# Kernel optimization log

Hardware: AMD Instinct MI355X
Metric: run time of the kernel (lower is better)

The kernel has to match this reference:

```python
import jax, jax.numpy as jnp
import numpy as np

B, T, C = 2, 2048, 1024
H, DH = 16, 64          # n_heads = d_model // 64
WIN = 256               # sliding window size
K = 32                  # n_oscillators
DFF = 4096              # d_ff_hidden
NEG = -1e9


def setup_inputs() -> dict:
    key = jax.random.key(0)
    ks = jax.random.split(key, 16)
    sC = 1.0 / np.sqrt(C)
    sF = 1.0 / np.sqrt(DFF)
    sK = 1.0 / np.sqrt(K)
    return {
        "x": jax.random.normal(ks[0], (B, T, C), jnp.float32),
        "norm1_w": jnp.ones((C,), jnp.float32),
        "qkv_w": jax.random.normal(ks[1], (3 * C, C), jnp.float32) * sC,
        "qkv_b": jnp.zeros((3 * C,), jnp.float32),
        "proj_w": jax.random.normal(ks[2], (C, C), jnp.float32) * sC,
        "proj_b": jnp.zeros((C,), jnp.float32),
        "gate_w": jax.random.normal(ks[3], (1, C), jnp.float32) * 0.01,
        "gate_b": jnp.zeros((1,), jnp.float32),
        "trn_win": jax.random.normal(ks[4], (K, C), jnp.float32) * sC,
        "trn_wout": jax.random.normal(ks[5], (C, K), jnp.float32) * sK,
        "trn_gate_w": jax.random.normal(ks[6], (K, C), jnp.float32) * sC,
        "trn_gate_b": jnp.zeros((K,), jnp.float32),
        "trn_a_logit": jax.random.normal(ks[7], (K,), jnp.float32),
        "trn_theta": jax.random.uniform(ks[8], (K,), jnp.float32, 0.0, np.pi),
        "trn_res_scale": jnp.asarray(0.1, jnp.float32),
        "norm2_w": jnp.ones((C,), jnp.float32),
        "ffn_gate_w": jax.random.normal(ks[9], (DFF, C), jnp.float32) * sC,
        "ffn_up_w": jax.random.normal(ks[10], (DFF, C), jnp.float32) * sC,
        "ffn_down_w": jax.random.normal(ks[11], (C, DFF), jnp.float32) * sF,
    }


def _rms(z, w, eps=1e-6):
    return z * jax.lax.rsqrt(jnp.mean(z * z, axis=-1, keepdims=True) + eps) * w


def reference(x, norm1_w, qkv_w, qkv_b, proj_w, proj_b, gate_w, gate_b,
              trn_win, trn_wout, trn_gate_w, trn_gate_b, trn_a_logit,
              trn_theta, trn_res_scale, norm2_w, ffn_gate_w, ffn_up_w,
              ffn_down_w):
    h = _rms(x, norm1_w)

    # ---- windowed causal attention (dense mask, as in the original) ----
    qkv = h @ qkv_w.T + qkv_b                       # [B,T,3C]
    q, k, v = jnp.split(qkv, 3, axis=-1)
    heads = lambda t: t.reshape(B, T, H, DH).transpose(0, 2, 1, 3)  # [B,H,T,DH]
    q, k, v = heads(q), heads(k), heads(v)
    row = jnp.arange(T)[:, None]
    col = jnp.arange(T)[None, :]
    mask = jnp.where((col <= row) & (col >= row - WIN + 1), 0.0, NEG).astype(x.dtype)
    scores = jnp.einsum('bhqd,bhkd->bhqk', q, k) / jnp.sqrt(jnp.asarray(DH, x.dtype))
    attn = jax.nn.softmax(scores + mask, axis=-1)
    ao = jnp.einsum('bhqk,bhkd->bhqd', attn, v).transpose(0, 2, 1, 3).reshape(B, T, C)
    ao = ao @ proj_w.T + proj_b

    # ---- temporal resonance branch: K damped rotating oscillators ----
    u = h @ trn_win.T                               # [B,T,K] drive
    a = jax.nn.sigmoid(trn_a_logit)                 # amplitude in (0,1) (amplitude_max=1)
    ct, st = jnp.cos(trn_theta), jnp.sin(trn_theta)

    def step(carry, ut):
        sr, si = carry
        nsr = a * (ct * sr - st * si) + ut
        nsi = a * (st * sr + ct * si)
        return (nsr, nsi), nsr

    init = (jnp.zeros((B, K), x.dtype), jnp.zeros((B, K), x.dtype))
    _, ys = jax.lax.scan(step, init, u.transpose(1, 0, 2))  # ys: [T,B,K]
    y = ys.transpose(1, 0, 2)                                # [B,T,K]
    tg = jax.nn.sigmoid(h @ trn_gate_w.T + trn_gate_b)
    trn_out = ((tg * y) @ trn_wout.T) * trn_res_scale        # [B,T,C]

    # ---- sigmoid gate mix + residual ----
    g = jax.nn.sigmoid(h @ gate_w.T + gate_b)       # [B,T,1]
    x = x + g * ao + (1.0 - g) * trn_out

    # ---- SwiGLU FFN ----
    h2 = _rms(x, norm2_w)
    ffn = (jax.nn.silu(h2 @ ffn_gate_w.T) * (h2 @ ffn_up_w.T)) @ ffn_down_w.T
    return x + ffn
```

## Files before the change

### kernel.cpp

```cpp
#include <hip/hip_runtime.h>


typedef unsigned short u16;
typedef unsigned short u16x8 __attribute__((ext_vector_type(8)));
typedef __bf16 bf16x8 __attribute__((ext_vector_type(8)));
typedef float f32x4 __attribute__((ext_vector_type(4)));

#define DI static __device__ __forceinline__

DI u16 f2b(float f){
  union { float f; unsigned u; } v; v.f = f;
  unsigned r = v.u + 0x7FFFu + ((v.u >> 16) & 1u);
  return (u16)(r >> 16);
}
DI float b2f(u16 b){
  union { unsigned u; float f; } v; v.u = ((unsigned)b) << 16; return v.f;
}
DI u16x8 ld8(const u16* p){ return *(const u16x8*)p; }

DI f32x4 MFMA16(u16x8 a, u16x8 b, f32x4 c){
  return __builtin_amdgcn_mfma_f32_16x16x32_bf16(
      __builtin_bit_cast(bf16x8, a), __builtin_bit_cast(bf16x8, b), c, 0, 0, 0);
}

DI void async16(const void* g, void* l){
  void* gg = const_cast<void*>(g);
  __builtin_amdgcn_global_load_lds(
      (__attribute__((address_space(1))) void*)gg,
      (__attribute__((address_space(3))) void*)l, 16, 0, 0);
}

__global__ __launch_bounds__(256) void convert_w(
    const float* __restrict__ qkvw, const float* __restrict__ projw,
    const float* __restrict__ fgw, const float* __restrict__ fuw,
    const float* __restrict__ fdw, const float* __restrict__ twin,
    const float* __restrict__ tgw, const float* __restrict__ twout,
    u16* __restrict__ dst)
{
  size_t i = (size_t)blockIdx.x * 256 + threadIdx.x;
  if (i >= 4235264u) return;
  size_t e = i * 4;
  float4 v;
  if (e < 3145728u)        v = *(const float4*)(qkvw + e);
  else if (e < 3276800u){
    size_t i2 = e - 3145728u;
    int row = (int)(i2 >> 10), c = (int)(i2 & 1023);
    if (row < 32)      v = *(const float4*)(twin + row * 1024 + c);
    else if (row < 64) v = *(const float4*)(tgw + (row - 32) * 1024 + c);
    else               v = make_float4(0.f, 0.f, 0.f, 0.f);
  }
  else if (e < 4325376u)   v = *(const float4*)(projw + (e - 3276800u));
  else if (e < 12713984u){
    size_t i2 = e - 4325376u;
    int row = (int)(i2 >> 10), c = (int)(i2 & 1023);
    int G = row >> 5, j = row & 31;
    const float* src = (j < 16) ? fgw : fuw;
    v = *(const float4*)(src + (size_t)(G * 16 + (j & 15)) * 1024 + c);
  }
  else if (e < 16908288u)  v = *(const float4*)(fdw + (e - 12713984u));
  else                     v = *(const float4*)(twout + (e - 16908288u));
  uint2 p;
  p.x = (unsigned)f2b(v.x) | ((unsigned)f2b(v.y) << 16);
  p.y = (unsigned)f2b(v.z) | ((unsigned)f2b(v.w) << 16);
  *(uint2*)(dst + e) = p;
}

__global__ __launch_bounds__(256) void rmsnorm_gate(
    const float* __restrict__ x, const float* __restrict__ w,
    const float* __restrict__ gw, const float* __restrict__ gb,
    u16* __restrict__ h, float* __restrict__ g)
{
  const int row = blockIdx.x, tid = threadIdx.x;
  const int wave = tid >> 6, lane = tid & 63;
  __shared__ float sb[8];
  float4 xv = ((const float4*)(x + (size_t)row * 1024))[tid];
  float ss = xv.x*xv.x + xv.y*xv.y + xv.z*xv.z + xv.w*xv.w;
#pragma unroll
  for (int m = 32; m; m >>= 1) ss += __shfl_xor(ss, m);
  if (lane == 0) sb[wave] = ss;
  __syncthreads();
  float rstd = rsqrtf((sb[0]+sb[1]+sb[2]+sb[3]) * (1.f/1024.f) + 1e-6f);
  float4 wv = ((const float4*)w)[tid];
  float h0 = xv.x*rstd*wv.x, h1 = xv.y*rstd*wv.y;
  float h2v = xv.z*rstd*wv.z, h3 = xv.w*rstd*wv.w;
  uint2 pk;
  pk.x = (unsigned)f2b(h0) | ((unsigned)f2b(h1) << 16);
  pk.y = (unsigned)f2b(h2v) | ((unsigned)f2b(h3) << 16);
  ((uint2*)(h + (size_t)row * 1024))[tid] = pk;
  float4 gv = ((const float4*)gw)[tid];
  float gd = h0*gv.x + h1*gv.y + h2v*gv.z + h3*gv.w;
#pragma unroll
  for (int m = 32; m; m >>= 1) gd += __shfl_xor(gd, m);
  if (lane == 0) sb[4 + wave] = gd;
  __syncthreads();
  if (tid == 0) g[row] = 1.f / (1.f + __expf(-(sb[4]+sb[5]+sb[6]+sb[7] + gb[0])));
}

__global__ __launch_bounds__(256) void reduce_mix_norm(
    const u16* __restrict__ part, const float* __restrict__ x,
    const u16* __restrict__ trn, const float* __restrict__ g,
    const float* __restrict__ pb, const float* __restrict__ n2w,
    float* __restrict__ out, u16* __restrict__ h2)
{
  const int row = blockIdx.x, tid = threadIdx.x;
  const int wave = tid >> 6, lane = tid & 63;
  __shared__ float sb[4];
  const size_t ro = (size_t)row * 1024;
  uint2 a0 = ((const uint2*)(part + ro))[tid];
  uint2 a1 = ((const uint2*)(part + 4194304 + ro))[tid];
  float4 bb = ((const float4*)pb)[tid];
  float4 xv = ((const float4*)(x + ro))[tid];
  uint2 tz = ((const uint2*)(trn + ro))[tid];
  float gg = g[row];
  float p00 = b2f((u16)a0.x), p01 = b2f((u16)(a0.x >> 16));
  float p02 = b2f((u16)a0.y), p03 = b2f((u16)(a0.y >> 16));
  float p10 = b2f((u16)a1.x), p11 = b2f((u16)(a1.x >> 16));
  float p12 = b2f((u16)a1.y), p13 = b2f((u16)(a1.y >> 16));
  float t0 = b2f((u16)tz.x), t1 = b2f((u16)(tz.x >> 16));
  float t2 = b2f((u16)tz.y), t3 = b2f((u16)(tz.y >> 16));
  float m0 = xv.x + gg*(p00+p10+bb.x) + (1.f-gg)*t0;
  float m1 = xv.y + gg*(p01+p11+bb.y) + (1.f-gg)*t1;
  float m2 = xv.z + gg*(p02+p12+bb.z) + (1.f-gg)*t2;
  float m3 = xv.w + gg*(p03+p13+bb.w) + (1.f-gg)*t3;
  float4 mo; mo.x = m0; mo.y = m1; mo.z = m2; mo.w = m3;
  ((float4*)(out + ro))[tid] = mo;
  float ss = m0*m0 + m1*m1 + m2*m2 + m3*m3;
#pragma unroll
  for (int m = 32; m; m >>= 1) ss += __shfl_xor(ss, m);
  if (lane == 0) sb[wave] = ss;
  __syncthreads();
  float rstd = rsqrtf((sb[0]+sb[1]+sb[2]+sb[3]) * (1.f/1024.f) + 1e-6f);
  float4 wv = ((const float4*)n2w)[tid];
  uint2 pk;
  pk.x = (unsigned)f2b(m0*rstd*wv.x) | ((unsigned)f2b(m1*rstd*wv.y) << 16);
  pk.y = (unsigned)f2b(m2*rstd*wv.z) | ((unsigned)f2b(m3*rstd*wv.w) << 16);
  ((uint2*)(h2 + ro))[tid] = pk;
}

__global__ __launch_bounds__(256) void reduce_down(
    const u16* __restrict__ part, float* __restrict__ out)
{
  size_t i = (size_t)blockIdx.x * 256 + threadIdx.x;
  uint2 a0 = ((const uint2*)part)[i];
  uint2 a1 = ((const uint2*)(part + 4194304))[i];
  float4 xv = ((float4*)out)[i];
  float4 o;
  o.x = xv.x + b2f((u16)a0.x) + b2f((u16)a1.x);
  o.y = xv.y + b2f((u16)(a0.x >> 16)) + b2f((u16)(a1.x >> 16));
  o.z = xv.z + b2f((u16)a0.y) + b2f((u16)a1.y);
  o.w = xv.w + b2f((u16)(a0.y >> 16)) + b2f((u16)(a1.y >> 16));
  ((float4*)out)[i] = o;
}

template<int MODE, bool WIDE>
__global__ __launch_bounds__(256) void gemm_bt(
    const u16* __restrict__ A, const u16* __restrict__ B,
    float* __restrict__ outF, float* __restrict__ outF2, u16* __restrict__ outB,
    const float* __restrict__ bias, const float* __restrict__ auxF,
    int M, int N, int K)
{
  __shared__ __align__(16) u16 sA[2][128 * 32];
  __shared__ __align__(16) u16 sB[2][128 * 32];
  const int tid = threadIdx.x;
  const int wave = tid >> 6, lane = tid & 63;
  const int lr = lane & 15, lq = lane >> 4;
  const int m0 = blockIdx.x * 128, n0 = blockIdx.y * 128;
  const int wm = (wave & 1) * 64, wn = (wave >> 1) * 64;
  const int ks = K / (int)gridDim.z;
  const int kbeg = (int)blockIdx.z * ks, kend = kbeg + ks;
  f32x4 acc[4][4] = {};
  const int srow = wave * 16 + (lane >> 2);
  const int scol = (lane & 3) * 8;
  const u16* gA = A + (size_t)(m0 + srow) * K + scol;
  const u16* gB = B + (size_t)(n0 + srow) * K + scol;
  u16* lA0 = &sA[0][(wave * 16) * 32];
  u16* lA1 = &sA[0][(64 + wave * 16) * 32];
  u16* lB0 = &sB[0][(wave * 16) * 32];
  u16* lB1 = &sB[0][(64 + wave * 16) * 32];
  const size_t K64 = (size_t)64 * K;
  const int BUF = 128 * 32;

  if (WIDE){
    for (int k0 = kbeg; k0 < kend; k0 += 64){
      async16(gA + k0,            lA0);
      async16(gA + K64 + k0,      lA1);
      async16(gB + k0,            lB0);
      async16(gB + K64 + k0,      lB1);
      async16(gA + k0 + 32,       lA0 + BUF);
      async16(gA + K64 + k0 + 32, lA1 + BUF);
      async16(gB + k0 + 32,       lB0 + BUF);
      async16(gB + K64 + k0 + 32, lB1 + BUF);
      __syncthreads();
      u16x8 af[4], bf[4];
#pragma unroll
      for (int i = 0; i < 4; i++) af[i] = ld8(&sA[0][(wm + i*16 + lr)*32 + lq*8]);
#pragma unroll
      for (int i = 0; i < 4; i++) bf[i] = ld8(&sB[0][(wn + i*16 + lr)*32 + lq*8]);
#pragma unroll
      for (int mi = 0; mi < 4; mi++)
#pragma unroll
        for (int ni = 0; ni < 4; ni++)
          acc[mi][ni] = MFMA16(af[mi], bf[ni], acc[mi][ni]);
#pragma unroll
      for (int i = 0; i < 4; i++) af[i] = ld8(&sA[1][(wm + i*16 + lr)*32 + lq*8]);
#pragma unroll
      for (int i = 0; i < 4; i++) bf[i] = ld8(&sB[1][(wn + i*16 + lr)*32 + lq*8]);
#pragma unroll
      for (int mi = 0; mi < 4; mi++)
#pragma unroll
        for (int ni = 0; ni < 4; ni++)
          acc[mi][ni] = MFMA16(af[mi], bf[ni], acc[mi][ni]);
      __syncthreads();
    }
  } else {
    for (int k0 = kbeg; k0 < kend; k0 += 32){
      async16(gA + k0,       lA0);
      async16(gA + K64 + k0, lA1);
      async16(gB + k0,       lB0);
      async16(gB + K64 + k0, lB1);
      __syncthreads();
      u16x8 af[4], bf[4];
#pragma unroll
      for (int i = 0; i < 4; i++) af[i] = ld8(&sA[0][(wm + i*16 + lr)*32 + lq*8]);
#pragma unroll
      for (int i = 0; i < 4; i++) bf[i] = ld8(&sB[0][(wn + i*16 + lr)*32 + lq*8]);
#pragma unroll
      for (int mi = 0; mi < 4; mi++)
#pragma unroll
        for (int ni = 0; ni < 4; ni++)
          acc[mi][ni] = MFMA16(af[mi], bf[ni], acc[mi][ni]);
      __syncthreads();
    }
  }

  if (MODE == 7){
    const int cb = ((n0 + wn) >> 1) + lr;
#pragma unroll
    for (int mi = 0; mi < 4; mi++){
      const int row = m0 + wm + mi*16 + lq*4;
#pragma unroll
      for (int p = 0; p < 2; p++){
        const int col = cb + p*16;
#pragma unroll
        for (int r = 0; r < 4; r++){
          float gv = acc[mi][2*p][r], uv = acc[mi][2*p+1][r];
          float rv = gv / (1.f + __expf(-gv)) * uv;
          outB[(size_t)(row + r) * (N >> 1) + col] = f2b(rv);
        }
      }
    }
    return;
  }

  float scale6 = 0.f;
  if (MODE == 6) scale6 = auxF[0];

#pragma unroll
  for (int mi = 0; mi < 4; mi++){
    const int row = m0 + wm + mi*16 + lq*4;
#pragma unroll
    for (int ni = 0; ni < 4; ni++){
      const int col = n0 + wn + ni*16 + lr;
#pragma unroll
      for (int r = 0; r < 4; r++){
        const int rr = row + r;
        float v = acc[mi][ni][r];
        if (MODE == 0){
          if (n0 < 3072){
            outB[(size_t)rr * 3072 + col] = f2b(v + bias[col]);
          } else {
            int c2 = col - 3072;
            int bb = rr >> 11, tt = rr & 2047;
            if (c2 < 32) outF[((size_t)bb * 32 + c2) * 2048 + tt] = v;
            else if (c2 < 64)
              outF2[(size_t)rr * 32 + (c2 - 32)] =
                  1.f / (1.f + __expf(-(v + auxF[c2 - 32])));
          }
        } else if (MODE == 6){
          outB[(size_t)rr * N + col] = f2b(v * scale6);
        } else if (MODE == 9){
          outB[(size_t)blockIdx.z * (size_t)M + (size_t)rr * N + col] = f2b(v);
        }
      }
    }
  }
}

__global__ __launch_bounds__(256) void attn_win(
    const u16* __restrict__ qkv, u16* __restrict__ ao)
{
  const int blk = blockIdx.x;
  const int tile = blk & 31, hh = (blk >> 5) & 15, b = blk >> 9;
  const int t0 = tile * 64;
  const int tid = threadIdx.x, wave = tid >> 6, lane = tid & 63;
  const int lr = lane & 15, lq = lane >> 4;
  const int qt = t0 + wave * 16;
  __shared__ __align__(16) u16 sVt[64 * 40];
  __shared__ __align__(16) u16 sP[4][16 * 32];

  const u16* base = qkv + (size_t)b * 2048 * 3072 + hh * 64;
  const u16* qrow = base + (size_t)(qt + lr) * 3072 + lq * 8;
  u16x8 qf0 = ld8(qrow), qf1 = ld8(qrow + 32);
  const u16* kbase = base + 1024;
  const u16* vbase = base + 2048;

  f32x4 o0 = {0,0,0,0}, o1 = {0,0,0,0}, o2 = {0,0,0,0}, o3 = {0,0,0,0};
  float lsum[4] = {0.f, 0.f, 0.f, 0.f};
  const float c1 = 0.125f * 1.44269504088896f;

  const int kb = (t0 >= 256) ? (t0 - 256) : 0;
  const int ntl = (t0 + 64 - kb) >> 5;
  for (int it = 0; it < ntl; ++it){
    const int kt = kb + it * 32;
    __syncthreads();
    {
      const int key = tid & 31, dseg = tid >> 5;
      const u16* gv = vbase + (size_t)(kt + key) * 3072 + dseg * 8;
      u16x8 v0 = ld8(gv);
#pragma unroll
      for (int j = 0; j < 8; j++)
        sVt[(dseg*8 + j) * 40 + key] = v0[j];
    }
    __syncthreads();
    const bool active = (kt < qt + 16) && (kt + 286 >= qt);
    if (!active) continue;

    f32x4 s0 = {0,0,0,0}, s1 = {0,0,0,0};
    {
      const u16* kr = kbase + (size_t)(kt + lr) * 3072 + lq * 8;
      u16x8 k00 = ld8(kr), k01 = ld8(kr + 32);
      const u16* kr1 = kr + (size_t)16 * 3072;
      u16x8 k10 = ld8(kr1), k11 = ld8(kr1 + 32);
      s0 = MFMA16(qf0, k00, s0); s0 = MFMA16(qf1, k01, s0);
      s1 = MFMA16(qf0, k10, s1); s1 = MFMA16(qf1, k11, s1);
    }
#pragma unroll
    for (int r = 0; r < 4; r++){
      const int q = qt + lq * 4 + r;
      const int ca = kt + lr, cb = kt + 16 + lr;
      float p0 = (ca <= q && ca + 255 >= q) ? exp2f(s0[r] * c1) : 0.f;
      float p1 = (cb <= q && cb + 255 >= q) ? exp2f(s1[r] * c1) : 0.f;
      lsum[r] += p0 + p1;
      sP[wave][(lq*4 + r) * 32 + lr]      = f2b(p0);
      sP[wave][(lq*4 + r) * 32 + 16 + lr] = f2b(p1);
    }
    __builtin_amdgcn_s_waitcnt(0xc07f);
    u16x8 pf = ld8(&sP[wave][lr * 32 + lq * 8]);
    o0 = MFMA16(pf, ld8(&sVt[(lr)      * 40 + lq * 8]), o0);
    o1 = MFMA16(pf, ld8(&sVt[(16 + lr) * 40 + lq * 8]), o1);
    o2 = MFMA16(pf, ld8(&sVt[(32 + lr) * 40 + lq * 8]), o2);
    o3 = MFMA16(pf, ld8(&sVt[(48 + lr) * 40 + lq * 8]), o3);
  }

#pragma unroll
  for (int r = 0; r < 4; r++){
    float l = lsum[r];
    l += __shfl_xor(l, 1); l += __shfl_xor(l, 2);
    l += __shfl_xor(l, 4); l += __shfl_xor(l, 8);
    lsum[r] = l;
  }

  u16* aor = ao + (size_t)(b * 2048 + qt + lq * 4) * 1024 + hh * 64 + lr;
#pragma unroll
  for (int r = 0; r < 4; r++){
    float inv = 1.f / lsum[r];
    u16* p = aor + (size_t)r * 1024;
    p[0]  = f2b(o0[r] * inv);
    p[16] = f2b(o1[r] * inv);
    p[32] = f2b(o2[r] * inv);
    p[48] = f2b(o3[r] * inv);
  }
}

__global__ __launch_bounds__(256) void scan_k(
    const float* __restrict__ u_t, const float* __restrict__ tg,
    const float* __restrict__ alog, const float* __restrict__ theta,
    u16* __restrict__ z)
{
  const int bk = blockIdx.x;
  const int b = bk >> 5, k = bk & 31;
  const int j = threadIdx.x;
  const float a = 1.f / (1.f + __expf(-alog[k]));
  const float th = theta[k];
  const float wr = a * __cosf(th), wi = a * __sinf(th);
  const float* ubp = u_t + ((size_t)b * 32 + k) * 2048 + j * 8;
  float4 ua = ((const float4*)ubp)[0];
  float4 ub4 = ((const float4*)ubp)[1];
  float ur[8] = {ua.x, ua.y, ua.z, ua.w, ub4.x, ub4.y, ub4.z, ub4.w};
  float sr = 0.f, si = 0.f;
#pragma unroll
  for (int i = 0; i < 8; i++){
    float nr = wr*sr - wi*si + ur[i];
    float ni = wi*sr + wr*si;
    sr = nr; si = ni;
  }
  float w2r = wr*wr - wi*wi, w2i = 2.f*wr*wi;
  float w4r = w2r*w2r - w2i*w2i, w4i = 2.f*w2r*w2i;
  float Ar = w4r*w4r - w4i*w4i, Ai = 2.f*w4r*w4i;
  __shared__ float4 sc[256];
  float4 cur; cur.x = Ar; cur.y = Ai; cur.z = sr; cur.w = si;
  sc[j] = cur;
  __syncthreads();
  for (int s = 1; s < 256; s <<= 1){
    float4 pv;
    const bool has = (j >= s);
    if (has) pv = sc[j - s];
    __syncthreads();
    if (has){
      float nar = cur.x*pv.x - cur.y*pv.y;
      float nai = cur.x*pv.y + cur.y*pv.x;
      float nbr = cur.x*pv.z - cur.y*pv.w + cur.z;
      float nbi = cur.x*pv.w + cur.y*pv.z + cur.w;
      cur.x = nar; cur.y = nai; cur.z = nbr; cur.w = nbi;
    }
    sc[j] = cur;
    __syncthreads();
  }
  float s_r = 0.f, s_i = 0.f;
  if (j > 0){ float4 pr = sc[j - 1]; s_r = pr.z; s_i = pr.w; }
  const float* tgp = tg + ((size_t)b * 2048 + j * 8) * 32 + k;
  u16* zp = z + ((size_t)b * 2048 + j * 8) * 32 + k;
#pragma unroll
  for (int i = 0; i < 8; i++){
    float nr = wr*s_r - wi*s_i + ur[i];
    float ni = wi*s_r + wr*s_i;
    s_r = nr; s_i = ni;
    zp[(size_t)i * 32] = f2b(s_r * tgp[(size_t)i * 32]);
  }
}

extern "C" void kernel_launch(void* const* d_in, const int* in_sizes, int n_in,
                              void* d_out, int out_size, void* d_ws, size_t ws_size,
                              hipStream_t stream)
{
  (void)in_sizes; (void)n_in; (void)out_size; (void)ws_size;
  const float* x      = (const float*)d_in[0];
  const float* n1w    = (const float*)d_in[1];
  const float* qkvw   = (const float*)d_in[2];
  const float* qkvb   = (const float*)d_in[3];
  const float* projw  = (const float*)d_in[4];
  const float* projb  = (const float*)d_in[5];
  const float* gatew  = (const float*)d_in[6];
  const float* gateb  = (const float*)d_in[7];
  const float* twin   = (const float*)d_in[8];
  const float* twout  = (const float*)d_in[9];
  const float* tgw    = (const float*)d_in[10];
  const float* tgb    = (const float*)d_in[11];
  const float* talog  = (const float*)d_in[12];
  const float* ttheta = (const float*)d_in[13];
  const float* tscale = (const float*)d_in[14];
  const float* n2w    = (const float*)d_in[15];
  const float* fgw    = (const float*)d_in[16];
  const float* fuw    = (const float*)d_in[17];
  const float* fdw    = (const float*)d_in[18];
  float* out = (float*)d_out;

  char* wsb = (char*)d_ws;
  size_t off = 0;
  auto take = [&](size_t bytes) -> void* {
    void* r = wsb + off; off += (bytes + 255) & ~(size_t)255; return r;
  };
  u16*   wall = (u16*)take(16941056ull * 2);
  u16*   h    = (u16*)take(4194304ull * 2);
  u16*   h2   = (u16*)take(4194304ull * 2);
  u16*   trn  = (u16*)take(4194304ull * 2);
  float* g    = (float*)take(4096ull * 4);
  float* u_t  = (float*)take(131072ull * 4);
  float* tg   = (float*)take(131072ull * 4);
  u16*   zz   = (u16*)take(131072ull * 2);
  u16*   regA = (u16*)take(4096ull * 4096 * 2);
  u16*   regB = (u16*)take(4096ull * 4096 * 2);

  u16* wq  = wall;
  u16* wp  = wall + 3276800;
  u16* wgu = wall + 4325376;
  u16* wd  = wall + 12713984;
  u16* wo  = wall + 16908288;
  u16* qkv    = regA;
  u16* pproj  = regA;
  u16* pdown  = regA;
  u16* ao     = regB;
  u16* act    = regB;

  convert_w<<<16544, 256, 0, stream>>>(qkvw, projw, fgw, fuw, fdw, twin, tgw, twout, wall);
  rmsnorm_gate<<<4096, 256, 0, stream>>>(x, n1w, gatew, gateb, h, g);
  gemm_bt<0, true><<<dim3(32, 25), 256, 0, stream>>>(h, wq, u_t, tg, qkv, qkvb,
                                                     tgb, 0, 3200, 1024);
  attn_win<<<1024, 256, 0, stream>>>(qkv, ao);
  scan_k<<<64, 256, 0, stream>>>(u_t, tg, talog, ttheta, zz);
  gemm_bt<6, false><<<dim3(32, 8), 256, 0, stream>>>(zz, wo, nullptr, nullptr, trn, nullptr,
                                                     tscale, 0, 1024, 32);
  gemm_bt<9, true><<<dim3(32, 8, 2), 256, 0, stream>>>(ao, wp, nullptr, nullptr, pproj,
                                                       nullptr, nullptr, 4194304, 1024, 1024);
  reduce_mix_norm<<<4096, 256, 0, stream>>>(pproj, x, trn, g, projb, n2w, out, h2);
  gemm_bt<7, true><<<dim3(32, 64), 256, 0, stream>>>(h2, wgu, nullptr, nullptr, act, nullptr,
                                                     nullptr, 0, 8192, 1024);
  gemm_bt<9, true><<<dim3(32, 8, 2), 256, 0, stream>>>(act, wd, nullptr, nullptr, pdown,
                                                       nullptr, nullptr, 4194304, 1024, 4096);
  reduce_down<<<4096, 256, 0, stream>>>(pdown, out);
}
```

Before: 418.5 us.

## Fold resonance output projection into proj GEMM and merge small kernels

The resonance output projection is folded into the attention projection GEMM. The gated attention output and the gated, scaled oscillator states are concatenated along K (1024+32, padded to 1152), and the weight matrix is built as [proj_w | trn_wout | 0]. This removes the separate trn GEMM, its bf16 intermediate buffer and its read in the mix kernel. Attention, scan and padding-zero work are merged into one launch, as are weight conversion and RMSNorm. The attention key tile grows from 32 to 64 keys. The costs are a larger K for the proj GEMM, extra masked-out key work at window edges, and the gate factor now applied before bf16 rounding.

```diff
diff --git a/kernel.cpp b/kernel.cpp
--- a/kernel.cpp
+++ b/kernel.cpp
@@ -30,47 +30,52 @@
       (__attribute__((address_space(3))) void*)l, 16, 0, 0);
 }
 
-__global__ __launch_bounds__(256) void convert_w(
+__global__ __launch_bounds__(256) void prep_kernel(
     const float* __restrict__ qkvw, const float* __restrict__ projw,
     const float* __restrict__ fgw, const float* __restrict__ fuw,
     const float* __restrict__ fdw, const float* __restrict__ twin,
     const float* __restrict__ tgw, const float* __restrict__ twout,
-    u16* __restrict__ dst)
-{
-  size_t i = (size_t)blockIdx.x * 256 + threadIdx.x;
-  if (i >= 4235264u) return;
-  size_t e = i * 4;
-  float4 v;
-  if (e < 3145728u)        v = *(const float4*)(qkvw + e);
-  else if (e < 3276800u){
-    size_t i2 = e - 3145728u;
-    int row = (int)(i2 >> 10), c = (int)(i2 & 1023);
-    if (row < 32)      v = *(const float4*)(twin + row * 1024 + c);
-    else if (row < 64) v = *(const float4*)(tgw + (row - 32) * 1024 + c);
-    else               v = make_float4(0.f, 0.f, 0.f, 0.f);
-  }
-  else if (e < 4325376u)   v = *(const float4*)(projw + (e - 3276800u));
-  else if (e < 12713984u){
-    size_t i2 = e - 4325376u;
-    int row = (int)(i2 >> 10), c = (int)(i2 & 1023);
-    int G = row >> 5, j = row & 31;
-    const float* src = (j < 16) ? fgw : fuw;
-    v = *(const float4*)(src + (size_t)(G * 16 + (j & 15)) * 1024 + c);
-  }
-  else if (e < 16908288u)  v = *(const float4*)(fdw + (e - 12713984u));
-  else                     v = *(const float4*)(twout + (e - 16908288u));
-  uint2 p;
-  p.x = (unsigned)f2b(v.x) | ((unsigned)f2b(v.y) << 16);
-  p.y = (unsigned)f2b(v.z) | ((unsigned)f2b(v.w) << 16);
-  *(uint2*)(dst + e) = p;
-}
-
-__global__ __launch_bounds__(256) void rmsnorm_gate(
-    const float* __restrict__ x, const float* __restrict__ w,
+    u16* __restrict__ dst,
+    const float* __restrict__ x, const float* __restrict__ n1w,
     const float* __restrict__ gw, const float* __restrict__ gb,
     u16* __restrict__ h, float* __restrict__ g)
 {
-  const int row = blockIdx.x, tid = threadIdx.x;
+  const int blk = blockIdx.x, tid = threadIdx.x;
+  if (blk < 16640){
+    size_t i = (size_t)blk * 256 + tid;
+    if (i >= 4259840u) return;
+    size_t e = i * 4;
+    float4 v;
+    if (e < 3145728u)        v = *(const float4*)(qkvw + e);
+    else if (e < 3276800u){
+      size_t i2 = e - 3145728u;
+      int row = (int)(i2 >> 10), c = (int)(i2 & 1023);
+      if (row < 32)      v = *(const float4*)(twin + row * 1024 + c);
+      else if (row < 64) v = *(const float4*)(tgw + (row - 32) * 1024 + c);
+      else               v = make_float4(0.f, 0.f, 0.f, 0.f);
+    }
+    else if (e < 4456448u){
+      unsigned i2 = (unsigned)(e - 3276800u);
+      unsigned row = i2 / 1152u, kk = i2 - row * 1152u;
+      if (kk < 1024u)      v = *(const float4*)(projw + (size_t)row * 1024 + kk);
+      else if (kk < 1056u) v = *(const float4*)(twout + (size_t)row * 32 + (kk - 1024u));
+      else                 v = make_float4(0.f, 0.f, 0.f, 0.f);
+    }
+    else if (e < 12845056u){
+      size_t i2 = e - 4456448u;
+      int row = (int)(i2 >> 10), c = (int)(i2 & 1023);
+      int G = row >> 5, j = row & 31;
+      const float* src = (j < 16) ? fgw : fuw;
+      v = *(const float4*)(src + (size_t)(G * 16 + (j & 15)) * 1024 + c);
+    }
+    else                   v = *(const float4*)(fdw + (e - 12845056u));
+    uint2 p;
+    p.x = (unsigned)f2b(v.x) | ((unsigned)f2b(v.y) << 16);
+    p.y = (unsigned)f2b(v.z) | ((unsigned)f2b(v.w) << 16);
+    *(uint2*)(dst + e) = p;
+    return;
+  }
+  const int row = blk - 16640;
   const int wave = tid >> 6, lane = tid & 63;
   __shared__ float sb[8];
   float4 xv = ((const float4*)(x + (size_t)row * 1024))[tid];
@@ -80,7 +85,7 @@
   if (lane == 0) sb[wave] = ss;
   __syncthreads();
   float rstd = rsqrtf((sb[0]+sb[1]+sb[2]+sb[3]) * (1.f/1024.f) + 1e-6f);
-  float4 wv = ((const float4*)w)[tid];
+  float4 wv = ((const float4*)n1w)[tid];
   float h0 = xv.x*rstd*wv.x, h1 = xv.y*rstd*wv.y;
   float h2v = xv.z*rstd*wv.z, h3 = xv.w*rstd*wv.w;
   uint2 pk;
@@ -98,8 +103,8 @@
 
 __global__ __launch_bounds__(256) void reduce_mix_norm(
     const u16* __restrict__ part, const float* __restrict__ x,
-    const u16* __restrict__ trn, const float* __restrict__ g,
-    const float* __restrict__ pb, const float* __restrict__ n2w,
+    const float* __restrict__ g, const float* __restrict__ pb,
+    const float* __restrict__ n2w,
     float* __restrict__ out, u16* __restrict__ h2)
 {
   const int row = blockIdx.x, tid = threadIdx.x;
@@ -110,18 +115,11 @@
   uint2 a1 = ((const uint2*)(part + 4194304 + ro))[tid];
   float4 bb = ((const float4*)pb)[tid];
   float4 xv = ((const float4*)(x + ro))[tid];
-  uint2 tz = ((const uint2*)(trn + ro))[tid];
   float gg = g[row];
-  float p00 = b2f((u16)a0.x), p01 = b2f((u16)(a0.x >> 16));
-  float p02 = b2f((u16)a0.y), p03 = b2f((u16)(a0.y >> 16));
-  float p10 = b2f((u16)a1.x), p11 = b2f((u16)(a1.x >> 16));
-  float p12 = b2f((u16)a1.y), p13 = b2f((u16)(a1.y >> 16));
-  float t0 = b2f((u16)tz.x), t1 = b2f((u16)(tz.x >> 16));
-  float t2 = b2f((u16)tz.y), t3 = b2f((u16)(tz.y >> 16));
-  float m0 = xv.x + gg*(p00+p10+bb.x) + (1.f-gg)*t0;
-  float m1 = xv.y + gg*(p01+p11+bb.y) + (1.f-gg)*t1;
-  float m2 = xv.z + gg*(p02+p12+bb.z) + (1.f-gg)*t2;
-  float m3 = xv.w + gg*(p03+p13+bb.w) + (1.f-gg)*t3;
+  float m0 = xv.x + b2f((u16)a0.x) + b2f((u16)a1.x) + gg*bb.x;
+  float m1 = xv.y + b2f((u16)(a0.x >> 16)) + b2f((u16)(a1.x >> 16)) + gg*bb.y;
+  float m2 = xv.z + b2f((u16)a0.y) + b2f((u16)a1.y) + gg*bb.z;
+  float m3 = xv.w + b2f((u16)(a0.y >> 16)) + b2f((u16)(a1.y >> 16)) + gg*bb.w;
   float4 mo; mo.x = m0; mo.y = m1; mo.z = m2; mo.w = m3;
   ((float4*)(out + ro))[tid] = mo;
   float ss = m0*m0 + m1*m1 + m2*m2 + m3*m3;
@@ -252,9 +250,6 @@
     return;
   }
 
-  float scale6 = 0.f;
-  if (MODE == 6) scale6 = auxF[0];
-
 #pragma unroll
   for (int mi = 0; mi < 4; mi++){
     const int row = m0 + wm + mi*16 + lq*4;
@@ -276,8 +271,6 @@
               outF2[(size_t)rr * 32 + (c2 - 32)] =
                   1.f / (1.f + __expf(-(v + auxF[c2 - 32])));
           }
-        } else if (MODE == 6){
-          outB[(size_t)rr * N + col] = f2b(v * scale6);
         } else if (MODE == 9){
           outB[(size_t)blockIdx.z * (size_t)M + (size_t)rr * N + col] = f2b(v);
         }
@@ -286,146 +279,168 @@
   }
 }
 
-__global__ __launch_bounds__(256) void attn_win(
-    const u16* __restrict__ qkv, u16* __restrict__ ao)
-{
-  const int blk = blockIdx.x;
-  const int tile = blk & 31, hh = (blk >> 5) & 15, b = blk >> 9;
-  const int t0 = tile * 64;
-  const int tid = threadIdx.x, wave = tid >> 6, lane = tid & 63;
-  const int lr = lane & 15, lq = lane >> 4;
-  const int qt = t0 + wave * 16;
-  __shared__ __align__(16) u16 sVt[64 * 40];
-  __shared__ __align__(16) u16 sP[4][16 * 32];
-
-  const u16* base = qkv + (size_t)b * 2048 * 3072 + hh * 64;
-  const u16* qrow = base + (size_t)(qt + lr) * 3072 + lq * 8;
-  u16x8 qf0 = ld8(qrow), qf1 = ld8(qrow + 32);
-  const u16* kbase = base + 1024;
-  const u16* vbase = base + 2048;
-
-  f32x4 o0 = {0,0,0,0}, o1 = {0,0,0,0}, o2 = {0,0,0,0}, o3 = {0,0,0,0};
-  float lsum[4] = {0.f, 0.f, 0.f, 0.f};
-  const float c1 = 0.125f * 1.44269504088896f;
-
-  const int kb = (t0 >= 256) ? (t0 - 256) : 0;
-  const int ntl = (t0 + 64 - kb) >> 5;
-  for (int it = 0; it < ntl; ++it){
-    const int kt = kb + it * 32;
-    __syncthreads();
-    {
-      const int key = tid & 31, dseg = tid >> 5;
-      const u16* gv = vbase + (size_t)(kt + key) * 3072 + dseg * 8;
-      u16x8 v0 = ld8(gv);
-#pragma unroll
-      for (int j = 0; j < 8; j++)
-        sVt[(dseg*8 + j) * 40 + key] = v0[j];
-    }
-    __syncthreads();
-    const bool active = (kt < qt + 16) && (kt + 286 >= qt);
-    if (!active) continue;
-
-    f32x4 s0 = {0,0,0,0}, s1 = {0,0,0,0};
-    {
-      const u16* kr = kbase + (size_t)(kt + lr) * 3072 + lq * 8;
-      u16x8 k00 = ld8(kr), k01 = ld8(kr + 32);
-      const u16* kr1 = kr + (size_t)16 * 3072;
-      u16x8 k10 = ld8(kr1), k11 = ld8(kr1 + 32);
-      s0 = MFMA16(qf0, k00, s0); s0 = MFMA16(qf1, k01, s0);
-      s1 = MFMA16(qf0, k10, s1); s1 = MFMA16(qf1, k11, s1);
-    }
-#pragma unroll
-    for (int r = 0; r < 4; r++){
-      const int q = qt + lq * 4 + r;
-      const int ca = kt + lr, cb = kt + 16 + lr;
-      float p0 = (ca <= q && ca + 255 >= q) ? exp2f(s0[r] * c1) : 0.f;
-      float p1 = (cb <= q && cb + 255 >= q) ? exp2f(s1[r] * c1) : 0.f;
-      lsum[r] += p0 + p1;
-      sP[wave][(lq*4 + r) * 32 + lr]      = f2b(p0);
-      sP[wave][(lq*4 + r) * 32 + 16 + lr] = f2b(p1);
-    }
-    __builtin_amdgcn_s_waitcnt(0xc07f);
-    u16x8 pf = ld8(&sP[wave][lr * 32 + lq * 8]);
-    o0 = MFMA16(pf, ld8(&sVt[(lr)      * 40 + lq * 8]), o0);
-    o1 = MFMA16(pf, ld8(&sVt[(16 + lr) * 40 + lq * 8]), o1);
-    o2 = MFMA16(pf, ld8(&sVt[(32 + lr) * 40 + lq * 8]), o2);
-    o3 = MFMA16(pf, ld8(&sVt[(48 + lr) * 40 + lq * 8]), o3);
-  }
-
-#pragma unroll
-  for (int r = 0; r < 4; r++){
-    float l = lsum[r];
-    l += __shfl_xor(l, 1); l += __shfl_xor(l, 2);
-    l += __shfl_xor(l, 4); l += __shfl_xor(l, 8);
-    lsum[r] = l;
-  }
-
-  u16* aor = ao + (size_t)(b * 2048 + qt + lq * 4) * 1024 + hh * 64 + lr;
-#pragma unroll
-  for (int r = 0; r < 4; r++){
-    float inv = 1.f / lsum[r];
-    u16* p = aor + (size_t)r * 1024;
-    p[0]  = f2b(o0[r] * inv);
-    p[16] = f2b(o1[r] * inv);
-    p[32] = f2b(o2[r] * inv);
-    p[48] = f2b(o3[r] * inv);
-  }
-}
-
-__global__ __launch_bounds__(256) void scan_k(
+__global__ __launch_bounds__(256) void attn_scan(
+    const u16* __restrict__ qkv, const float* __restrict__ g,
     const float* __restrict__ u_t, const float* __restrict__ tg,
     const float* __restrict__ alog, const float* __restrict__ theta,
-    u16* __restrict__ z)
+    const float* __restrict__ tscale, u16* __restrict__ Ap)
 {
-  const int bk = blockIdx.x;
-  const int b = bk >> 5, k = bk & 31;
-  const int j = threadIdx.x;
-  const float a = 1.f / (1.f + __expf(-alog[k]));
-  const float th = theta[k];
-  const float wr = a * __cosf(th), wi = a * __sinf(th);
-  const float* ubp = u_t + ((size_t)b * 32 + k) * 2048 + j * 8;
-  float4 ua = ((const float4*)ubp)[0];
-  float4 ub4 = ((const float4*)ubp)[1];
-  float ur[8] = {ua.x, ua.y, ua.z, ua.w, ub4.x, ub4.y, ub4.z, ub4.w};
-  float sr = 0.f, si = 0.f;
-#pragma unroll
-  for (int i = 0; i < 8; i++){
-    float nr = wr*sr - wi*si + ur[i];
-    float ni = wi*sr + wr*si;
-    sr = nr; si = ni;
-  }
-  float w2r = wr*wr - wi*wi, w2i = 2.f*wr*wi;
-  float w4r = w2r*w2r - w2i*w2i, w4i = 2.f*w2r*w2i;
-  float Ar = w4r*w4r - w4i*w4i, Ai = 2.f*w4r*w4i;
+  __shared__ __align__(16) u16 sVt[64 * 72];
+  __shared__ __align__(16) u16 sP[4][16 * 72];
   __shared__ float4 sc[256];
-  float4 cur; cur.x = Ar; cur.y = Ai; cur.z = sr; cur.w = si;
-  sc[j] = cur;
-  __syncthreads();
-  for (int s = 1; s < 256; s <<= 1){
-    float4 pv;
-    const bool has = (j >= s);
-    if (has) pv = sc[j - s];
-    __syncthreads();
-    if (has){
-      float nar = cur.x*pv.x - cur.y*pv.y;
-      float nai = cur.x*pv.y + cur.y*pv.x;
-      float nbr = cur.x*pv.z - cur.y*pv.w + cur.z;
-      float nbi = cur.x*pv.w + cur.y*pv.z + cur.w;
-      cur.x = nar; cur.y = nai; cur.z = nbr; cur.w = nbi;
-    }
+  const int blk = blockIdx.x, tid = threadIdx.x;
+
+  if (blk < 1024){
+    const int tile = blk & 31, hh = (blk >> 5) & 15, b = blk >> 9;
+    const int t0 = tile * 64;
+    const int wave = tid >> 6, lane = tid & 63;
+    const int lr = lane & 15, lq = lane >> 4;
+    const int qt = t0 + wave * 16;
+
+    const u16* base = qkv + (size_t)b * 2048 * 3072 + hh * 64;
+    const u16* qrow = base + (size_t)(qt + lr) * 3072 + lq * 8;
+    u16x8 qf0 = ld8(qrow), qf1 = ld8(qrow + 32);
+    const u16* kbase = base + 1024;
+    const u16* vbase = base + 2048;
+
+    f32x4 o0 = {0,0,0,0}, o1 = {0,0,0,0}, o2 = {0,0,0,0}, o3 = {0,0,0,0};
+    float lsum[4] = {0.f, 0.f, 0.f, 0.f};
+    const float c1 = 0.125f * 1.44269504088896f;
+
+    const int kb = (t0 >= 256) ? (t0 - 256) : 0;
+    const int ntl = (t0 + 64 - kb) >> 6;
+    for (int it = 0; it < ntl; ++it){
+      const int kt = kb + it * 64;
+      __syncthreads();
+      {
+        const int key = tid & 63, dseg = tid >> 6;
+        const u16* gv = vbase + (size_t)(kt + key) * 3072 + dseg * 16;
+        u16x8 v0 = ld8(gv), v1 = ld8(gv + 8);
+#pragma unroll
+        for (int j = 0; j < 8; j++){
+          sVt[(dseg*16 + j)     * 72 + key] = v0[j];
+          sVt[(dseg*16 + 8 + j) * 72 + key] = v1[j];
+        }
+      }
+      __syncthreads();
+      const bool active = (kt < qt + 16) && (kt + 318 >= qt);
+      if (!active) continue;
+
+      f32x4 s[4] = {};
+#pragma unroll
+      for (int gK = 0; gK < 4; gK++){
+        const u16* kr = kbase + (size_t)(kt + gK*16 + lr) * 3072 + lq * 8;
+        u16x8 k0 = ld8(kr), k1 = ld8(kr + 32);
+        s[gK] = MFMA16(qf0, k0, s[gK]);
+        s[gK] = MFMA16(qf1, k1, s[gK]);
+      }
+#pragma unroll
+      for (int r = 0; r < 4; r++){
+        const int q = qt + lq * 4 + r;
+#pragma unroll
+        for (int gK = 0; gK < 4; gK++){
+          const int c = kt + gK*16 + lr;
+          float p = (c <= q && c + 255 >= q) ? exp2f(s[gK][r] * c1) : 0.f;
+          lsum[r] += p;
+          sP[wave][(lq*4 + r) * 72 + gK*16 + lr] = f2b(p);
+        }
+      }
+      __builtin_amdgcn_s_waitcnt(0xc07f);
+      u16x8 pf0 = ld8(&sP[wave][lr * 72 + lq * 8]);
+      u16x8 pf1 = ld8(&sP[wave][lr * 72 + 32 + lq * 8]);
+      o0 = MFMA16(pf0, ld8(&sVt[(lr)      * 72 + lq * 8]), o0);
+      o0 = MFMA16(pf1, ld8(&sVt[(lr)      * 72 + 32 + lq * 8]), o0);
+      o1 = MFMA16(pf0, ld8(&sVt[(16 + lr) * 72 + lq * 8]), o1);
+      o1 = MFMA16(pf1, ld8(&sVt[(16 + lr) * 72 + 32 + lq * 8]), o1);
+      o2 = MFMA16(pf0, ld8(&sVt[(32 + lr) * 72 + lq * 8]), o2);
+      o2 = MFMA16(pf1, ld8(&sVt[(32 + lr) * 72 + 32 + lq * 8]), o2);
+      o3 = MFMA16(pf0, ld8(&sVt[(48 + lr) * 72 + lq * 8]), o3);
+      o3 = MFMA16(pf1, ld8(&sVt[(48 + lr) * 72 + 32 + lq * 8]), o3);
+    }
+
+#pragma unroll
+    for (int r = 0; r < 4; r++){
+      float l = lsum[r];
+      l += __shfl_xor(l, 1); l += __shfl_xor(l, 2);
+      l += __shfl_xor(l, 4); l += __shfl_xor(l, 8);
+      lsum[r] = l;
+    }
+
+    const int trow = b * 2048 + qt + lq * 4;
+    u16* aor = Ap + (size_t)trow * 1152 + hh * 64 + lr;
+#pragma unroll
+    for (int r = 0; r < 4; r++){
+      float inv = g[trow + r] / lsum[r];
+      u16* p = aor + (size_t)r * 1152;
+      p[0]  = f2b(o0[r] * inv);
+      p[16] = f2b(o1[r] * inv);
+      p[32] = f2b(o2[r] * inv);
+      p[48] = f2b(o3[r] * inv);
+    }
+    return;
+  }
+
+  if (blk < 1088){
+    const int bk = blk - 1024;
+    const int b = bk >> 5, k = bk & 31;
+    const int j = tid;
+    const float a = 1.f / (1.f + __expf(-alog[k]));
+    const float th = theta[k];
+    const float rs = tscale[0];
+    const float wr = a * __cosf(th), wi = a * __sinf(th);
+    const float* ubp = u_t + ((size_t)b * 32 + k) * 2048 + j * 8;
+    float4 ua = ((const float4*)ubp)[0];
+    float4 ub4 = ((const float4*)ubp)[1];
+    float ur[8] = {ua.x, ua.y, ua.z, ua.w, ub4.x, ub4.y, ub4.z, ub4.w};
+    float sr = 0.f, si = 0.f;
+#pragma unroll
+    for (int i = 0; i < 8; i++){
+      float nr = wr*sr - wi*si + ur[i];
+      float ni = wi*sr + wr*si;
+      sr = nr; si = ni;
+    }
+    float w2r = wr*wr - wi*wi, w2i = 2.f*wr*wi;
+    float w4r = w2r*w2r - w2i*w2i, w4i = 2.f*w2r*w2i;
+    float Ar = w4r*w4r - w4i*w4i, Ai = 2.f*w4r*w4i;
+    float4 cur; cur.x = Ar; cur.y = Ai; cur.z = sr; cur.w = si;
     sc[j] = cur;
     __syncthreads();
-  }
-  float s_r = 0.f, s_i = 0.f;
-  if (j > 0){ float4 pr = sc[j - 1]; s_r = pr.z; s_i = pr.w; }
-  const float* tgp = tg + ((size_t)b * 2048 + j * 8) * 32 + k;
-  u16* zp = z + ((size_t)b * 2048 + j * 8) * 32 + k;
-#pragma unroll
-  for (int i = 0; i < 8; i++){
-    float nr = wr*s_r - wi*s_i + ur[i];
-    float ni = wi*s_r + wr*s_i;
-    s_r = nr; s_i = ni;
-    zp[(size_t)i * 32] = f2b(s_r * tgp[(size_t)i * 32]);
+    for (int s = 1; s < 256; s <<= 1){
+      float4 pv;
+      const bool has = (j >= s);
+      if (has) pv = sc[j - s];
+      __syncthreads();
+      if (has){
+        float nar = cur.x*pv.x - cur.y*pv.y;
+        float nai = cur.x*pv.y + cur.y*pv.x;
+        float nbr = cur.x*pv.z - cur.y*pv.w + cur.z;
+        float nbi = cur.x*pv.w + cur.y*pv.z + cur.w;
+        cur.x = nar; cur.y = nai; cur.z = nbr; cur.w = nbi;
+      }
+      sc[j] = cur;
+      __syncthreads();
+    }
+    float s_r = 0.f, s_i = 0.f;
+    if (j > 0){ float4 pr = sc[j - 1]; s_r = pr.z; s_i = pr.w; }
+    const int bt0 = b * 2048 + j * 8;
+    const float* tgp = tg + (size_t)bt0 * 32 + k;
+    u16* zp = Ap + (size_t)bt0 * 1152 + 1024 + k;
+#pragma unroll
+    for (int i = 0; i < 8; i++){
+      float nr = wr*s_r - wi*s_i + ur[i];
+      float ni = wi*s_r + wr*s_i;
+      s_r = nr; s_i = ni;
+      float sc2 = (1.f - g[bt0 + i]) * rs;
+      zp[(size_t)i * 1152] = f2b(s_r * tgp[(size_t)i * 32] * sc2);
+    }
+    return;
+  }
+
+  {
+    unsigned idx = (unsigned)(blk - 1088) * 256 + tid;
+    unsigned row = idx / 12u, seg = idx - row * 12u;
+    uint4 z4; z4.x = 0; z4.y = 0; z4.z = 0; z4.w = 0;
+    *(uint4*)(Ap + (size_t)row * 1152 + 1056 + seg * 8) = z4;
   }
 }
 
@@ -460,39 +475,33 @@
   auto take = [&](size_t bytes) -> void* {
     void* r = wsb + off; off += (bytes + 255) & ~(size_t)255; return r;
   };
-  u16*   wall = (u16*)take(16941056ull * 2);
+  u16*   wall = (u16*)take(17039360ull * 2);
   u16*   h    = (u16*)take(4194304ull * 2);
   u16*   h2   = (u16*)take(4194304ull * 2);
-  u16*   trn  = (u16*)take(4194304ull * 2);
   float* g    = (float*)take(4096ull * 4);
   float* u_t  = (float*)take(131072ull * 4);
   float* tg   = (float*)take(131072ull * 4);
-  u16*   zz   = (u16*)take(131072ull * 2);
   u16*   regA = (u16*)take(4096ull * 4096 * 2);
   u16*   regB = (u16*)take(4096ull * 4096 * 2);
 
   u16* wq  = wall;
-  u16* wp  = wall + 3276800;
-  u16* wgu = wall + 4325376;
-  u16* wd  = wall + 12713984;
-  u16* wo  = wall + 16908288;
+  u16* wpx = wall + 3276800;
+  u16* wgu = wall + 4456448;
+  u16* wd  = wall + 12845056;
   u16* qkv    = regA;
   u16* pproj  = regA;
   u16* pdown  = regA;
-  u16* ao     = regB;
+  u16* Ap     = regB;
   u16* act    = regB;
 
-  convert_w<<<16544, 256, 0, stream>>>(qkvw, projw, fgw, fuw, fdw, twin, tgw, twout, wall);
-  rmsnorm_gate<<<4096, 256, 0, stream>>>(x, n1w, gatew, gateb, h, g);
+  prep_kernel<<<20736, 256, 0, stream>>>(qkvw, projw, fgw, fuw, fdw, twin, tgw,
+                                         twout, wall, x, n1w, gatew, gateb, h, g);
   gemm_bt<0, true><<<dim3(32, 25), 256, 0, stream>>>(h, wq, u_t, tg, qkv, qkvb,
                                                      tgb, 0, 3200, 1024);
-  attn_win<<<1024, 256, 0, stream>>>(qkv, ao);
-  scan_k<<<64, 256, 0, stream>>>(u_t, tg, talog, ttheta, zz);
-  gemm_bt<6, false><<<dim3(32, 8), 256, 0, stream>>>(zz, wo, nullptr, nullptr, trn, nullptr,
-                                                     tscale, 0, 1024, 32);
-  gemm_bt<9, true><<<dim3(32, 8, 2), 256, 0, stream>>>(ao, wp, nullptr, nullptr, pproj,
-                                                       nullptr, nullptr, 4194304, 1024, 1024);
-  reduce_mix_norm<<<4096, 256, 0, stream>>>(pproj, x, trn, g, projb, n2w, out, h2);
+  attn_scan<<<1280, 256, 0, stream>>>(qkv, g, u_t, tg, talog, ttheta, tscale, Ap);
+  gemm_bt<9, true><<<dim3(32, 8, 2), 256, 0, stream>>>(Ap, wpx, nullptr, nullptr, pproj,
+                                                       nullptr, nullptr, 4194304, 1024, 1152);
+  reduce_mix_norm<<<4096, 256, 0, stream>>>(pproj, x, g, projb, n2w, out, h2);
   gemm_bt<7, true><<<dim3(32, 64), 256, 0, stream>>>(h2, wgu, nullptr, nullptr, act, nullptr,
                                                      nullptr, 0, 8192, 1024);
   gemm_bt<9, true><<<dim3(32, 8, 2), 256, 0, stream>>>(act, wd, nullptr, nullptr, pdown,
```

After: 401.4 us. -4.1%, faster.
